# Performance work log

Hardware: AMD Instinct MI355X
Metric: run time of the kernel (lower is better)

Reference implementation:

```python
import jax, jax.numpy as jnp
import numpy as np


def _conv(x, w, stride, padding):
    # x: [N, Cin, H, W], w: [Cout, Cin, kh, kw]
    return jax.lax.conv_general_dilated(
        x, w, window_strides=(stride, stride), padding=padding,
        dimension_numbers=("NCHW", "OIHW", "NCHW"))


def _reflect_pad1(x):
    return jnp.pad(x, ((0, 0), (0, 0), (1, 1), (1, 1)), mode="reflect")


def setup_inputs() -> dict:
    key = jax.random.key(0)
    k1, k2, k3, k4 = jax.random.split(key, 4)
    B, C, H, W = 16, 3, 512, 512
    NC = 20  # num_channels (intermediate width)
    # xavier-uniform-like scales
    x = jax.random.normal(k1, (B, C, H, W), dtype=jnp.float32)
    w1 = jax.random.normal(k2, (NC, 1, 4, 4), dtype=jnp.float32) * (6.0 / (1 * 16 + NC * 16)) ** 0.5
    w2 = jax.random.normal(k3, (NC, NC, 4, 4), dtype=jnp.float32) * (6.0 / (NC * 16 + NC * 16)) ** 0.5
    w3 = jax.random.normal(k4, (1, NC, 3, 3), dtype=jnp.float32) * (6.0 / (NC * 9 + 1 * 9)) ** 0.5
    return {"x": x, "w1": w1, "w2": w2, "w3": w3}


def reference(x, w1, w2, w3):
    # Original torch code loops over input channels; equivalently fold the
    # channel dim into the batch dim and run the whole pipeline once.
    B, C, H, W = x.shape
    xr = x.reshape(B * C, 1, H, W)
    # stage 1: reflect pad 1 + 4x4 stride-2 conv + relu
    o1 = jax.nn.relu(_conv(_reflect_pad1(xr), w1, 2, "VALID"))  # [B*C, NC, 256, 256]
    # stage 2: reflect pad 1 + 4x4 stride-2 conv + relu
    o2 = jax.nn.relu(_conv(_reflect_pad1(o1), w2, 2, "VALID"))  # [B*C, NC, 128, 128]
    # stage 3: 3x3 conv, zero padding 1, + relu -> 1 channel per input channel
    o3 = jax.nn.relu(_conv(o2, w3, 1, ((1, 1), (1, 1))))        # [B*C, 1, 128, 128]
    Ho, Wo = o3.shape[-2], o3.shape[-1]
    return o3.reshape(B, C, Ho, Wo)
```

## Files before the change

kernel.cpp:

```cpp
#include <hip/hip_runtime.h>


#define NC 20
#define TS 12
#define OT 14
#define AR 16
#define SO1 48
#define PS1 770
#define SO2 16
#define PS2 226

#define W2F_OFF 256
#define W3_OFF  5376
#define WP_N    5556

typedef _Float16 h2  __attribute__((ext_vector_type(2)));
typedef __fp16   hq2 __attribute__((ext_vector_type(2)));
typedef _Float16 h8  __attribute__((ext_vector_type(8)));
typedef float    f32x16 __attribute__((ext_vector_type(16)));

__device__ __forceinline__ float dot2(unsigned int a, unsigned int b, float c) {
    return __builtin_amdgcn_fdot2(__builtin_bit_cast(h2, a),
                                  __builtin_bit_cast(h2, b), c, false);
}
__device__ __forceinline__ unsigned int packh(float a, float b) {
    _Float16 ha = (_Float16)a, hb = (_Float16)b;
    return (unsigned int)__builtin_bit_cast(unsigned short, ha) |
           ((unsigned int)__builtin_bit_cast(unsigned short, hb) << 16);
}
__device__ __forceinline__ unsigned int pkrtz(float a, float b) {
    hq2 r = __builtin_amdgcn_cvt_pkrtz(a, b);
    return __builtin_bit_cast(unsigned int, r);
}
__device__ __forceinline__ unsigned short f2h(float a) {
    _Float16 h = (_Float16)a;
    return __builtin_bit_cast(unsigned short, h);
}
__device__ __forceinline__ int refl256(int q) {
    q = (q < 0) ? -q : q; return (q > 255) ? 510 - q : q;
}
__device__ __forceinline__ int refl512(int q) {
    q = (q < 0) ? -q : q; return (q > 511) ? 1022 - q : q;
}

__global__ __launch_bounds__(256) void pack_weights(
    const float* __restrict__ w1, const float* __restrict__ w2,
    const float* __restrict__ w3, unsigned int* __restrict__ wp)
{
    const int i = blockIdx.x * 256 + threadIdx.x;
    if (i >= WP_N) return;
    if (i < W2F_OFF) {
        const int lane = i >> 2, jp = i & 3;
        const int ch = lane & 31, k0 = (lane >> 5) * 8 + 2 * jp;
        wp[i] = (ch < NC) ? packh(w1[ch * 16 + k0], w1[ch * 16 + k0 + 1]) : 0u;
    } else if (i < W3_OFF) {
        const int t = i - W2F_OFF;
        const int cin = t >> 8, r = t & 255;
        const int lane = r >> 2, jp = r & 3;
        const int cout = lane & 31, k0 = (lane >> 5) * 8 + 2 * jp;
        wp[i] = (cout < NC) ? packh(w2[(cout * NC + cin) * 16 + k0],
                                    w2[(cout * NC + cin) * 16 + k0 + 1]) : 0u;
    } else {
        const int t = i - W3_OFF;
        const int c = t / 9;
        const int r = t - c * 9;
        const int di = r / 3, wh = r - di * 3;
        const float* row = w3 + c * 9 + di * 3;
        float a, b;
        if (wh == 0)      { a = row[0]; b = row[1]; }
        else if (wh == 1) { a = row[2]; b = 0.f;    }
        else              { a = 0.f;    b = row[2]; }
        wp[i] = packh(a, b);
    }
}

__global__ __launch_bounds__(256, 4) void ds_fused(
    const float* __restrict__ x,
    const unsigned int* __restrict__ wp,
    float* __restrict__ out)
{
    __shared__ __attribute__((aligned(16))) unsigned short s_o1[NC * PS1];
    __shared__ __attribute__((aligned(16))) unsigned short s_o2[NC * PS2];

    const int bid  = blockIdx.x;
    const int img  = bid / 121;
    const int t121 = bid - img * 121;
    const int ty   = t121 / 11;
    const int tx   = t121 - ty * 11;
    const int y0   = ty * TS;
    const int x0   = tx * TS;
    const int tid  = threadIdx.x;
    const int lane = tid & 63;
    const int wv   = tid >> 6;
    const int l31  = lane & 31;
    const int kh   = lane >> 5;

    const float* __restrict__ xi = x + (size_t)img * (512 * 512);
    const uint4* __restrict__ w1f = (const uint4*)wp;
    const uint4* __restrict__ w2f = (const uint4*)(wp + W2F_OFF);
    const unsigned int* __restrict__ w3p = wp + W3_OFF;

    const int t0 = 2 * y0 - 2;
    const int s0 = 2 * x0 - 2;

    const int sA = s0 + l31;
    const bool edgeT = (tx == 0) || (tx == 10);
    const int vb = 2 * sA - 3;
    int v0 = 0, v1 = 0, v2 = 0, v3 = 0;
    if (edgeT) {
        const int n2 = refl256(sA - 1);
        const int vbb = 2 * n2 - 1;
        v0 = refl512(vbb);     v1 = refl512(vbb + 1);
        v2 = refl512(vbb + 2); v3 = refl512(vbb + 3);
    }
    const h8 w1frag = __builtin_bit_cast(h8, w1f[lane]);

    const int q  = 32 * wv + l31;
    const int qc = (q < 98) ? q : 0;
    const int li = (qc * 2341) >> 15;
    const int jl = qc - li * 14;
    const int offA = (2 * li + 2 * kh) * SO1 + 2 * jl;

    #pragma unroll
    for (int h = 0; h < 2; ++h) {
        for (int c = wv; c < AR; c += 4) {
            const int t = t0 + 14 * h + c;
            const int mrow = refl256(t - 1);
            const int rb = 2 * mrow - 1;
            const float* r0 = xi + refl512(rb)     * 512;
            const float* r1 = xi + refl512(rb + 1) * 512;
            const float* r2 = xi + refl512(rb + 2) * 512;
            const float* r3 = xi + refl512(rb + 3) * 512;
            const float* plo = kh ? r2 : r0;
            const float* phi = kh ? r3 : r1;
            float f0, f1, f2, f3, f4, f5, f6, f7;
            if (!edgeT) {
                const float* a0 = plo + vb;
                f0 = a0[0]; f1 = a0[1]; f2 = a0[2]; f3 = a0[3];
                const float* a1 = phi + vb;
                f4 = a1[0]; f5 = a1[1]; f6 = a1[2]; f7 = a1[3];
            } else {
                f0 = plo[v0]; f1 = plo[v1]; f2 = plo[v2]; f3 = plo[v3];
                f4 = phi[v0]; f5 = phi[v1]; f6 = phi[v2]; f7 = phi[v3];
            }
            uint4 aw;
            aw.x = pkrtz(f0, f1); aw.y = pkrtz(f2, f3);
            aw.z = pkrtz(f4, f5); aw.w = pkrtz(f6, f7);
            f32x16 o = {};
            o = __builtin_amdgcn_mfma_f32_32x32x16_f16(
                    __builtin_bit_cast(h8, aw), w1frag, o, 0, 0, 0);
            if (l31 < NC) {
                unsigned int* wr =
                    (unsigned int*)&s_o1[l31 * PS1 + c * SO1 + 4 * kh];
                wr[0]  = pkrtz(fmaxf(o[0],  0.f), fmaxf(o[1],  0.f));
                wr[1]  = pkrtz(fmaxf(o[2],  0.f), fmaxf(o[3],  0.f));
                wr[4]  = pkrtz(fmaxf(o[4],  0.f), fmaxf(o[5],  0.f));
                wr[5]  = pkrtz(fmaxf(o[6],  0.f), fmaxf(o[7],  0.f));
                wr[8]  = pkrtz(fmaxf(o[8],  0.f), fmaxf(o[9],  0.f));
                wr[9]  = pkrtz(fmaxf(o[10], 0.f), fmaxf(o[11], 0.f));
                wr[12] = pkrtz(fmaxf(o[12], 0.f), fmaxf(o[13], 0.f));
                wr[13] = pkrtz(fmaxf(o[14], 0.f), fmaxf(o[15], 0.f));
            }
        }
        __syncthreads();

        f32x16 acc = {};
        #pragma unroll
        for (int cin = 0; cin < NC; ++cin) {
            const uint4 bw = w2f[cin * 64 + lane];
            const unsigned short* pA = &s_o1[cin * PS1 + offA];
            uint4 aw;
            aw.x = *(const unsigned int*)(pA);
            aw.y = *(const unsigned int*)(pA + 2);
            aw.z = *(const unsigned int*)(pA + SO1);
            aw.w = *(const unsigned int*)(pA + SO1 + 2);
            acc = __builtin_amdgcn_mfma_f32_32x32x16_f16(
                      __builtin_bit_cast(h8, aw),
                      __builtin_bit_cast(h8, bw), acc, 0, 0, 0);
        }

        if (l31 < NC) {
            #pragma unroll
            for (int p = 0; p < 16; ++p) {
                const int mr  = (p & 3) + 8 * (p >> 2) + 4 * kh;
                const int qq  = 32 * wv + mr;
                if (qq < 98) {
                    const int li2 = (qq * 2341) >> 15;
                    const int jl2 = qq - li2 * 14;
                    const int ilt = 7 * h + li2;
                    const int oi  = y0 - 1 + ilt, oj = x0 - 1 + jl2;
                    const bool val = (oi >= 0) && (oi < 128) &&
                                     (oj >= 0) && (oj < 128);
                    s_o2[l31 * PS2 + ilt * SO2 + jl2] =
                        val ? f2h(fmaxf(acc[p], 0.f)) : (unsigned short)0;
                }
            }
        }
        __syncthreads();
    }

    if (tid < TS * TS) {
        const int oy = tid / TS;
        const int ox = tid - oy * TS;
        const int e  = ox & ~1;
        const int par = ox & 1;
        float accc = 0.f;
        for (int c = 0; c < NC; ++c) {
            #pragma unroll
            for (int di = 0; di < 3; ++di) {
                const unsigned int* row =
                    (const unsigned int*)&s_o2[c * PS2 + (oy + di) * SO2 + e];
                const unsigned int d0 = row[0];
                const unsigned int d1 = row[1];
                const unsigned int mm = __builtin_amdgcn_perm(d1, d0, 0x05040302u);
                const unsigned int u0 = par ? mm : d0;
                const unsigned int wa = w3p[c * 9 + di * 3 + 0];
                const unsigned int wb = w3p[c * 9 + di * 3 + 1];
                const unsigned int wc = w3p[c * 9 + di * 3 + 2];
                accc = dot2(u0, wa, accc);
                accc = dot2(d1, par ? wc : wb, accc);
            }
        }
        const int gy = y0 + oy, gx = x0 + ox;
        if (gy < 128 && gx < 128)
            out[(size_t)img * (128 * 128) + gy * 128 + gx] = fmaxf(accc, 0.f);
    }
}

extern "C" void kernel_launch(void* const* d_in, const int* in_sizes, int n_in,
                              void* d_out, int out_size, void* d_ws, size_t ws_size,
                              hipStream_t stream) {
    const float* x  = (const float*)d_in[0];
    const float* w1 = (const float*)d_in[1];
    const float* w2 = (const float*)d_in[2];
    const float* w3 = (const float*)d_in[3];
    unsigned int* wp = (unsigned int*)d_ws;
    float* out = (float*)d_out;
    pack_weights<<<dim3((WP_N + 255) / 256), dim3(256), 0, stream>>>(w1, w2, w3, wp);
    ds_fused<<<dim3(48 * 121), dim3(256), 0, stream>>>(x, wp, out);
}
```

Baseline: 178.6 us.

## Prefetch second half input taps into registers and skip reflect math on interior tiles

Input loads for both halves of the stage-1 tile are hoisted into register arrays. The second half's global loads are issued before the first half's stage-2 MFMA loop so their latency overlaps that compute. Row reflection arithmetic and stage-2 boundary masking are skipped for interior tiles, and the barriers are rearranged to match. This raises register pressure (32 extra live VGPRs) under a launch bound of 4 blocks, which may cause spills or reduce occupancy.

```diff
diff --git a/kernel.cpp b/kernel.cpp
--- a/kernel.cpp
+++ b/kernel.cpp
@@ -3,7 +3,6 @@
 
 #define NC 20
 #define TS 12
-#define OT 14
 #define AR 16
 #define SO1 48
 #define PS1 770
@@ -74,6 +73,40 @@
     }
 }
 
+__device__ __forceinline__ void load_taps(
+    const float* __restrict__ xi, int t0, int h, int wv, int kh,
+    bool rowEdge, bool colEdge, int vb, int v0, int v1, int v2, int v3,
+    unsigned int xw[4][4])
+{
+    #pragma unroll
+    for (int i = 0; i < 4; ++i) {
+        const int c = wv + 4 * i;
+        const int t = t0 + 14 * h + c;
+        int rlo, rhi;
+        if (!rowEdge) {
+            rlo = 2 * t - 3 + 2 * kh;
+            rhi = rlo + 1;
+        } else {
+            const int mr = refl256(t - 1);
+            const int rb = 2 * mr - 1 + 2 * kh;
+            rlo = refl512(rb);
+            rhi = refl512(rb + 1);
+        }
+        const float* __restrict__ plo = xi + rlo * 512;
+        const float* __restrict__ phi = xi + rhi * 512;
+        float f0, f1, f2, f3, f4, f5, f6, f7;
+        if (!colEdge) {
+            f0 = plo[vb]; f1 = plo[vb + 1]; f2 = plo[vb + 2]; f3 = plo[vb + 3];
+            f4 = phi[vb]; f5 = phi[vb + 1]; f6 = phi[vb + 2]; f7 = phi[vb + 3];
+        } else {
+            f0 = plo[v0]; f1 = plo[v1]; f2 = plo[v2]; f3 = plo[v3];
+            f4 = phi[v0]; f5 = phi[v1]; f6 = phi[v2]; f7 = phi[v3];
+        }
+        xw[i][0] = pkrtz(f0, f1); xw[i][1] = pkrtz(f2, f3);
+        xw[i][2] = pkrtz(f4, f5); xw[i][3] = pkrtz(f6, f7);
+    }
+}
+
 __global__ __launch_bounds__(256, 4) void ds_fused(
     const float* __restrict__ x,
     const unsigned int* __restrict__ wp,
@@ -104,10 +137,12 @@
     const int s0 = 2 * x0 - 2;
 
     const int sA = s0 + l31;
-    const bool edgeT = (tx == 0) || (tx == 10);
+    const bool rowEdge = (ty == 0) || (ty == 10);
+    const bool colEdge = (tx == 0) || (tx == 10);
+    const bool interior = !rowEdge && !colEdge;
     const int vb = 2 * sA - 3;
     int v0 = 0, v1 = 0, v2 = 0, v3 = 0;
-    if (edgeT) {
+    if (colEdge) {
         const int n2 = refl256(sA - 1);
         const int vbb = 2 * n2 - 1;
         v0 = refl512(vbb);     v1 = refl512(vbb + 1);
@@ -121,45 +156,57 @@
     const int jl = qc - li * 14;
     const int offA = (2 * li + 2 * kh) * SO1 + 2 * jl;
 
+    unsigned int xw0[4][4];
+    load_taps(xi, t0, 0, wv, kh, rowEdge, colEdge, vb, v0, v1, v2, v3, xw0);
+
+    #pragma unroll
+    for (int i = 0; i < 4; ++i) {
+        const int c = wv + 4 * i;
+        uint4 aw; aw.x = xw0[i][0]; aw.y = xw0[i][1];
+                  aw.z = xw0[i][2]; aw.w = xw0[i][3];
+        f32x16 o = {};
+        o = __builtin_amdgcn_mfma_f32_32x32x16_f16(
+                __builtin_bit_cast(h8, aw), w1frag, o, 0, 0, 0);
+        if (l31 < NC) {
+            unsigned int* wr = (unsigned int*)&s_o1[l31 * PS1 + c * SO1 + 4 * kh];
+            wr[0]  = pkrtz(fmaxf(o[0],  0.f), fmaxf(o[1],  0.f));
+            wr[1]  = pkrtz(fmaxf(o[2],  0.f), fmaxf(o[3],  0.f));
+            wr[4]  = pkrtz(fmaxf(o[4],  0.f), fmaxf(o[5],  0.f));
+            wr[5]  = pkrtz(fmaxf(o[6],  0.f), fmaxf(o[7],  0.f));
+            wr[8]  = pkrtz(fmaxf(o[8],  0.f), fmaxf(o[9],  0.f));
+            wr[9]  = pkrtz(fmaxf(o[10], 0.f), fmaxf(o[11], 0.f));
+            wr[12] = pkrtz(fmaxf(o[12], 0.f), fmaxf(o[13], 0.f));
+            wr[13] = pkrtz(fmaxf(o[14], 0.f), fmaxf(o[15], 0.f));
+        }
+    }
+
+    unsigned int xw1[4][4];
+    load_taps(xi, t0, 1, wv, kh, rowEdge, colEdge, vb, v0, v1, v2, v3, xw1);
+
     #pragma unroll
     for (int h = 0; h < 2; ++h) {
-        for (int c = wv; c < AR; c += 4) {
-            const int t = t0 + 14 * h + c;
-            const int mrow = refl256(t - 1);
-            const int rb = 2 * mrow - 1;
-            const float* r0 = xi + refl512(rb)     * 512;
-            const float* r1 = xi + refl512(rb + 1) * 512;
-            const float* r2 = xi + refl512(rb + 2) * 512;
-            const float* r3 = xi + refl512(rb + 3) * 512;
-            const float* plo = kh ? r2 : r0;
-            const float* phi = kh ? r3 : r1;
-            float f0, f1, f2, f3, f4, f5, f6, f7;
-            if (!edgeT) {
-                const float* a0 = plo + vb;
-                f0 = a0[0]; f1 = a0[1]; f2 = a0[2]; f3 = a0[3];
-                const float* a1 = phi + vb;
-                f4 = a1[0]; f5 = a1[1]; f6 = a1[2]; f7 = a1[3];
-            } else {
-                f0 = plo[v0]; f1 = plo[v1]; f2 = plo[v2]; f3 = plo[v3];
-                f4 = phi[v0]; f5 = phi[v1]; f6 = phi[v2]; f7 = phi[v3];
-            }
-            uint4 aw;
-            aw.x = pkrtz(f0, f1); aw.y = pkrtz(f2, f3);
-            aw.z = pkrtz(f4, f5); aw.w = pkrtz(f6, f7);
-            f32x16 o = {};
-            o = __builtin_amdgcn_mfma_f32_32x32x16_f16(
-                    __builtin_bit_cast(h8, aw), w1frag, o, 0, 0, 0);
-            if (l31 < NC) {
-                unsigned int* wr =
-                    (unsigned int*)&s_o1[l31 * PS1 + c * SO1 + 4 * kh];
-                wr[0]  = pkrtz(fmaxf(o[0],  0.f), fmaxf(o[1],  0.f));
-                wr[1]  = pkrtz(fmaxf(o[2],  0.f), fmaxf(o[3],  0.f));
-                wr[4]  = pkrtz(fmaxf(o[4],  0.f), fmaxf(o[5],  0.f));
-                wr[5]  = pkrtz(fmaxf(o[6],  0.f), fmaxf(o[7],  0.f));
-                wr[8]  = pkrtz(fmaxf(o[8],  0.f), fmaxf(o[9],  0.f));
-                wr[9]  = pkrtz(fmaxf(o[10], 0.f), fmaxf(o[11], 0.f));
-                wr[12] = pkrtz(fmaxf(o[12], 0.f), fmaxf(o[13], 0.f));
-                wr[13] = pkrtz(fmaxf(o[14], 0.f), fmaxf(o[15], 0.f));
+        if (h == 1) {
+            __syncthreads();
+            #pragma unroll
+            for (int i = 0; i < 4; ++i) {
+                const int c = wv + 4 * i;
+                uint4 aw; aw.x = xw1[i][0]; aw.y = xw1[i][1];
+                          aw.z = xw1[i][2]; aw.w = xw1[i][3];
+                f32x16 o = {};
+                o = __builtin_amdgcn_mfma_f32_32x32x16_f16(
+                        __builtin_bit_cast(h8, aw), w1frag, o, 0, 0, 0);
+                if (l31 < NC) {
+                    unsigned int* wr =
+                        (unsigned int*)&s_o1[l31 * PS1 + c * SO1 + 4 * kh];
+                    wr[0]  = pkrtz(fmaxf(o[0],  0.f), fmaxf(o[1],  0.f));
+                    wr[1]  = pkrtz(fmaxf(o[2],  0.f), fmaxf(o[3],  0.f));
+                    wr[4]  = pkrtz(fmaxf(o[4],  0.f), fmaxf(o[5],  0.f));
+                    wr[5]  = pkrtz(fmaxf(o[6],  0.f), fmaxf(o[7],  0.f));
+                    wr[8]  = pkrtz(fmaxf(o[8],  0.f), fmaxf(o[9],  0.f));
+                    wr[9]  = pkrtz(fmaxf(o[10], 0.f), fmaxf(o[11], 0.f));
+                    wr[12] = pkrtz(fmaxf(o[12], 0.f), fmaxf(o[13], 0.f));
+                    wr[13] = pkrtz(fmaxf(o[14], 0.f), fmaxf(o[15], 0.f));
+                }
             }
         }
         __syncthreads();
@@ -182,22 +229,26 @@
         if (l31 < NC) {
             #pragma unroll
             for (int p = 0; p < 16; ++p) {
-                const int mr  = (p & 3) + 8 * (p >> 2) + 4 * kh;
-                const int qq  = 32 * wv + mr;
+                const int mr = (p & 3) + 8 * (p >> 2) + 4 * kh;
+                const int qq = 32 * wv + mr;
                 if (qq < 98) {
                     const int li2 = (qq * 2341) >> 15;
                     const int jl2 = qq - li2 * 14;
                     const int ilt = 7 * h + li2;
-                    const int oi  = y0 - 1 + ilt, oj = x0 - 1 + jl2;
-                    const bool val = (oi >= 0) && (oi < 128) &&
-                                     (oj >= 0) && (oj < 128);
-                    s_o2[l31 * PS2 + ilt * SO2 + jl2] =
-                        val ? f2h(fmaxf(acc[p], 0.f)) : (unsigned short)0;
+                    if (interior) {
+                        s_o2[l31 * PS2 + ilt * SO2 + jl2] = f2h(fmaxf(acc[p], 0.f));
+                    } else {
+                        const int oi = y0 - 1 + ilt, oj = x0 - 1 + jl2;
+                        const bool val = (oi >= 0) && (oi < 128) &&
+                                         (oj >= 0) && (oj < 128);
+                        s_o2[l31 * PS2 + ilt * SO2 + jl2] =
+                            val ? f2h(fmaxf(acc[p], 0.f)) : (unsigned short)0;
+                    }
                 }
             }
         }
-        __syncthreads();
-    }
+    }
+    __syncthreads();
 
     if (tid < TS * TS) {
         const int oy = tid / TS;
```

Result: faster. 168.3 us (-5.8%).
